# Optimization experiments

Hardware: AMD Instinct MI355X
Metric: run time of the kernel (lower is better)

The kernel has to match this reference:

```python
import jax, jax.numpy as jnp
import numpy as np


def setup_inputs() -> dict:
    key = jax.random.key(0)
    ks = jax.random.split(key, 8)
    B, C, T = 8, 512, 2048
    Cq = C // 8
    s = 0.02
    return {
        "x": jax.random.normal(ks[0], (B, C, T), dtype=jnp.float32),
        "wq": jax.random.normal(ks[1], (Cq, C), dtype=jnp.float32) * s,
        "bq": jax.random.normal(ks[2], (Cq,), dtype=jnp.float32) * s,
        "wk": jax.random.normal(ks[3], (Cq, C), dtype=jnp.float32) * s,
        "bk": jax.random.normal(ks[4], (Cq,), dtype=jnp.float32) * s,
        "wv": jax.random.normal(ks[5], (C, C), dtype=jnp.float32) * s,
        "bv": jax.random.normal(ks[6], (C,), dtype=jnp.float32) * s,
        "gamma": jax.random.normal(ks[7], (1,), dtype=jnp.float32) * s,
    }


def reference(x, wq, bq, wk, bk, wv, bv, gamma):
    # x: [B, C, T]; conv1d with kernel_size=1 == per-timestep linear over channels
    q = jnp.einsum('oc,bct->bto', wq, x) + bq          # [B, T, Cq]
    k = jnp.einsum('oc,bct->bot', wk, x) + bk[None, :, None]  # [B, Cq, T]
    v = jnp.einsum('oc,bct->bto', wv, x) + bv          # [B, T, C]
    attn = jnp.einsum('bto,bos->bts', q, k)            # [B, T, T] (unscaled)
    attn = jax.nn.softmax(attn, axis=-1)
    out = jnp.einsum('bts,bsc->bct', attn, v)          # [B, C, T]
    return gamma[0] * out + x
```

## Files before the change

kernel.cpp:

```cpp
#include <hip/hip_runtime.h>


#define B_ 8
#define C_ 512
#define T_ 2048

typedef __attribute__((ext_vector_type(4))) float f32x4;
typedef __attribute__((ext_vector_type(8))) short bf16x8;
typedef unsigned short u16;
typedef unsigned int u32;

__device__ __forceinline__ u16 f2bf(float f) {
  u32 u = __float_as_uint(f);
  u += 0x7fffu + ((u >> 16) & 1);
  return (u16)(u >> 16);
}
__device__ __forceinline__ float bf2f(u16 h) {
  return __uint_as_float(((u32)h) << 16);
}

extern "C" __global__ __launch_bounds__(256)
void k_wcvt(const float* __restrict__ wq, const float* __restrict__ wk,
            const float* __restrict__ wv, u16* __restrict__ W) {
  int i = blockIdx.x * 256 + threadIdx.x;
  const float* src; u16* dst;
  if (i < 8192)       { src = wq + (size_t)i * 4;            dst = W + (size_t)i * 4; }
  else if (i < 16384) { int j = i - 8192;  src = wk + (size_t)j * 4; dst = W + 32768 + (size_t)j * 4; }
  else                { int j = i - 16384; src = wv + (size_t)j * 4; dst = W + 65536 + (size_t)j * 4; }
  float4 f = *(const float4*)src;
  ushort4 o;
  o.x = f2bf(f.x); o.y = f2bf(f.y); o.z = f2bf(f.z); o.w = f2bf(f.w);
  *(ushort4*)dst = o;
}

extern "C" __global__ __launch_bounds__(256)
void k_xpose(const float* __restrict__ x, u16* __restrict__ xT) {
  __shared__ alignas(16) u16 lds[64 * 72];
  const int tid = threadIdx.x;
  const int t0 = blockIdx.x * 64;
  const int c0 = blockIdx.y * 64;
  const int b  = blockIdx.z;
  const int cr = tid >> 2, tq = tid & 3;
  const float* xp = x + ((size_t)(b * C_ + c0 + cr)) * T_ + t0 + tq * 16;
  u16 vals[16];
#pragma unroll
  for (int q = 0; q < 4; q++) {
    float4 f = *(const float4*)(xp + q * 4);
    vals[q * 4 + 0] = f2bf(f.x);
    vals[q * 4 + 1] = f2bf(f.y);
    vals[q * 4 + 2] = f2bf(f.z);
    vals[q * 4 + 3] = f2bf(f.w);
  }
#pragma unroll
  for (int j = 0; j < 16; j++) lds[(tq * 16 + j) * 72 + cr] = vals[j];
  __syncthreads();
  const int tr = tid >> 2, cq = tid & 3;
  uint4 oa = *(const uint4*)&lds[tr * 72 + cq * 16];
  uint4 ob = *(const uint4*)&lds[tr * 72 + cq * 16 + 8];
  u16* op = xT + ((size_t)(b * T_ + t0 + tr)) * C_ + c0 + cq * 16;
  *(uint4*)op = oa;
  *(uint4*)(op + 8) = ob;
}

extern "C" __global__ __launch_bounds__(256)
void k_qk(const u16* __restrict__ xT, const u16* __restrict__ W,
          const float* __restrict__ bq, const float* __restrict__ bk,
          u16* __restrict__ QK) {
  const int tid = threadIdx.x;
  const int wave = tid >> 6, lane = tid & 63;
  const int quad = lane >> 4, l15 = lane & 15;
  const int id = blockIdx.x;
  const int b  = id & 7;
  const int t0 = (id >> 3) * 32;
  const int n0 = wave * 32;
  f32x4 acc[2][2];
#pragma unroll
  for (int i = 0; i < 2; i++)
#pragma unroll
    for (int j = 0; j < 2; j++) acc[i][j] = (f32x4){0.f, 0.f, 0.f, 0.f};
#pragma unroll
  for (int ks = 0; ks < 16; ks++) {
    bf16x8 af[2], bf[2];
#pragma unroll
    for (int mt = 0; mt < 2; mt++)
      af[mt] = *(const bf16x8*)(xT + ((size_t)(b * T_ + t0 + mt * 16 + l15)) * C_ +
                                ks * 32 + quad * 8);
#pragma unroll
    for (int ntl = 0; ntl < 2; ntl++) {
      const int n = n0 + ntl * 16 + l15;
      const u16* wrow = (n < 64) ? (W + (size_t)n * C_)
                                 : (W + 32768 + (size_t)(n - 64) * C_);
      bf[ntl] = *(const bf16x8*)(wrow + ks * 32 + quad * 8);
    }
#pragma unroll
    for (int mt = 0; mt < 2; mt++)
#pragma unroll
      for (int ntl = 0; ntl < 2; ntl++)
        acc[mt][ntl] = __builtin_amdgcn_mfma_f32_16x16x32_bf16(af[mt], bf[ntl],
                                                               acc[mt][ntl], 0, 0, 0);
  }
#pragma unroll
  for (int ntl = 0; ntl < 2; ntl++) {
    const int n = n0 + ntl * 16 + l15;
    const float bias = (n < 64) ? bq[n] : bk[n - 64];
#pragma unroll
    for (int mt = 0; mt < 2; mt++)
#pragma unroll
      for (int r = 0; r < 4; r++) {
        const int t = t0 + mt * 16 + quad * 4 + r;
        QK[((size_t)(b * T_ + t)) * 128 + n] = f2bf(acc[mt][ntl][r] + bias);
      }
  }
}

extern "C" __global__ __launch_bounds__(256)
void k_vt(const u16* __restrict__ xT, const u16* __restrict__ Wv,
          const float* __restrict__ bv, u16* __restrict__ VT) {
  const int tid = threadIdx.x;
  const int wave = tid >> 6, lane = tid & 63;
  const int quad = lane >> 4, l15 = lane & 15;
  const int id = blockIdx.x;
  const int b   = id & 7;
  const int slot = id >> 3;
  const int tt0 = (slot & 15) * 128;
  const int c00 = (slot >> 4) * 128;
  const int wm = (wave >> 1) * 64, wn = (wave & 1) * 64;
  f32x4 acc[4][4];
#pragma unroll
  for (int i = 0; i < 4; i++)
#pragma unroll
    for (int j = 0; j < 4; j++) acc[i][j] = (f32x4){0.f, 0.f, 0.f, 0.f};

  bf16x8 af[2][4], bfr[2][4];
  auto ldst = [&](int ks, int s) {
#pragma unroll
    for (int mt = 0; mt < 4; mt++)
      af[s][mt] = *(const bf16x8*)(Wv + ((size_t)(c00 + wm + mt * 16 + l15)) * C_ +
                                   ks * 32 + quad * 8);
#pragma unroll
    for (int nt = 0; nt < 4; nt++)
      bfr[s][nt] = *(const bf16x8*)(xT + ((size_t)(b * T_ + tt0 + wn + nt * 16 + l15)) * C_ +
                                    ks * 32 + quad * 8);
  };
  ldst(0, 0);
#pragma unroll
  for (int ks = 0; ks < 16; ks++) {
    const int cur = ks & 1;
    if (ks < 15) ldst(ks + 1, cur ^ 1);
#pragma unroll
    for (int mt = 0; mt < 4; mt++)
#pragma unroll
      for (int nt = 0; nt < 4; nt++)
        acc[mt][nt] = __builtin_amdgcn_mfma_f32_16x16x32_bf16(af[cur][mt], bfr[cur][nt],
                                                              acc[mt][nt], 0, 0, 0);
  }
#pragma unroll
  for (int mt = 0; mt < 4; mt++) {
#pragma unroll
    for (int r = 0; r < 4; r++) {
      const int c = c00 + wm + mt * 16 + quad * 4 + r;
      const float bias = bv[c];
#pragma unroll
      for (int nt = 0; nt < 4; nt++) {
        const int t = tt0 + wn + nt * 16 + l15;
        VT[((size_t)(b * C_ + c)) * T_ + t] = f2bf(acc[mt][nt][r] + bias);
      }
    }
  }
}

extern "C" __global__ __launch_bounds__(256)
void k_attn(const u16* __restrict__ QK, const u16* __restrict__ VT,
            const float* __restrict__ x, const float* __restrict__ gamma,
            float* __restrict__ out) {
  __shared__ alignas(16) u16 Vt[2][256 * 40];
  __shared__ alignas(16) u16 Kt[2][32 * 72];
  __shared__ alignas(16) u16 Pscr[4][32 * 40];

  const int tid = threadIdx.x;
  const int wave = tid >> 6, lane = tid & 63;
  const int quad = lane >> 4, l15 = lane & 15;
  const int id = blockIdx.x;
  const int b  = id & 7;
  const int slot = id >> 3;
  const int c0 = (slot >> 5) * 256;
  const int t0 = (slot & 31) * 64;
  const int wt = wave & 1;
  const int wc = wave >> 1;

  bf16x8 qa[2][2];
#pragma unroll
  for (int mt = 0; mt < 2; mt++) {
    const u16* qp = QK + ((size_t)(b * T_ + t0 + wt * 32 + mt * 16 + l15)) * 128 + quad * 8;
    qa[mt][0] = *(const bf16x8*)qp;
    qa[mt][1] = *(const bf16x8*)(qp + 32);
  }
  f32x4 acc[2][8];
#pragma unroll
  for (int i = 0; i < 2; i++)
#pragma unroll
    for (int j = 0; j < 8; j++) acc[i][j] = (f32x4){0.f, 0.f, 0.f, 0.f};
  float lacc[2][4] = {{0.f, 0.f, 0.f, 0.f}, {0.f, 0.f, 0.f, 0.f}};

  const u16* vbase = VT + ((size_t)(b * C_ + c0)) * T_;
  const u16* kbase = QK + ((size_t)b * T_) * 128 + 64;
  const int vrow = tid >> 2, vch = tid & 3;
  const int krow = tid >> 3, kch = tid & 7;
  uint4 vreg[4];
  uint4 kreg;

  auto gl_tiles = [&](int s0) {
#pragma unroll
    for (int r = 0; r < 4; r++)
      vreg[r] = *(const uint4*)(vbase + ((size_t)(vrow + 64 * r)) * T_ + s0 + vch * 8);
    kreg = *(const uint4*)(kbase + ((size_t)(s0 + krow)) * 128 + kch * 8);
  };
  auto st_tiles = [&](int par) {
#pragma unroll
    for (int r = 0; r < 4; r++)
      *(uint4*)&Vt[par][(vrow + 64 * r) * 40 + vch * 8] = vreg[r];
    *(uint4*)&Kt[par][krow * 72 + kch * 8] = kreg;
  };

  gl_tiles(0);
  st_tiles(0);
  __syncthreads();

  for (int i = 0; i < 64; i++) {
    const int par = i & 1;
    if (i < 63) gl_tiles((i + 1) * 32);

    f32x4 sacc[2][2];
#pragma unroll
    for (int mt = 0; mt < 2; mt++)
#pragma unroll
      for (int nt = 0; nt < 2; nt++) sacc[mt][nt] = (f32x4){0.f, 0.f, 0.f, 0.f};
#pragma unroll
    for (int nt = 0; nt < 2; nt++)
#pragma unroll
      for (int ks = 0; ks < 2; ks++) {
        bf16x8 kb = *(const bf16x8*)&Kt[par][(nt * 16 + l15) * 72 + ks * 32 + quad * 8];
#pragma unroll
        for (int mt = 0; mt < 2; mt++)
          sacc[mt][nt] = __builtin_amdgcn_mfma_f32_16x16x32_bf16(qa[mt][ks], kb,
                                                                sacc[mt][nt], 0, 0, 0);
      }

#pragma unroll
    for (int mt = 0; mt < 2; mt++)
#pragma unroll
      for (int nt = 0; nt < 2; nt++)
#pragma unroll
        for (int r = 0; r < 4; r++) {
          float p = __expf(sacc[mt][nt][r]);
          u16 h = f2bf(p);
          lacc[mt][r] += bf2f(h);
          Pscr[wave][(mt * 16 + quad * 4 + r) * 40 + nt * 16 + l15] = h;
        }
    bf16x8 pa[2];
#pragma unroll
    for (int mt = 0; mt < 2; mt++)
      pa[mt] = *(const bf16x8*)&Pscr[wave][(mt * 16 + l15) * 40 + quad * 8];

#pragma unroll
    for (int nt = 0; nt < 8; nt++) {
      bf16x8 vb = *(const bf16x8*)&Vt[par][(wc * 128 + nt * 16 + l15) * 40 + quad * 8];
#pragma unroll
      for (int mt = 0; mt < 2; mt++)
        acc[mt][nt] = __builtin_amdgcn_mfma_f32_16x16x32_bf16(pa[mt], vb,
                                                              acc[mt][nt], 0, 0, 0);
    }

    if (i < 63) st_tiles(par ^ 1);
    __syncthreads();
  }

#pragma unroll
  for (int mt = 0; mt < 2; mt++)
#pragma unroll
    for (int r = 0; r < 4; r++) {
      float v = lacc[mt][r];
      v += __shfl_xor(v, 1);
      v += __shfl_xor(v, 2);
      v += __shfl_xor(v, 4);
      v += __shfl_xor(v, 8);
      lacc[mt][r] = v;
    }

  const float g = gamma[0];
#pragma unroll
  for (int mt = 0; mt < 2; mt++) {
#pragma unroll
    for (int r = 0; r < 4; r++) {
      const int t = t0 + wt * 32 + mt * 16 + quad * 4 + r;
      const float sc = g / lacc[mt][r];
#pragma unroll
      for (int nt = 0; nt < 8; nt++) {
        const int c = c0 + wc * 128 + nt * 16 + l15;
        const size_t idx = ((size_t)(b * C_ + c)) * T_ + t;
        out[idx] = acc[mt][nt][r] * sc + x[idx];
      }
    }
  }
}

extern "C" void kernel_launch(void* const* d_in, const int* in_sizes, int n_in,
                              void* d_out, int out_size, void* d_ws, size_t ws_size,
                              hipStream_t stream) {
  (void)in_sizes; (void)n_in; (void)out_size; (void)ws_size;
  const float* x  = (const float*)d_in[0];
  const float* wq = (const float*)d_in[1];
  const float* bq = (const float*)d_in[2];
  const float* wk = (const float*)d_in[3];
  const float* bk = (const float*)d_in[4];
  const float* wv = (const float*)d_in[5];
  const float* bv = (const float*)d_in[6];
  const float* gm = (const float*)d_in[7];
  float* out = (float*)d_out;

  u16* xT = (u16*)d_out;
  u16* Wb = (u16*)((char*)d_out + (size_t)17 * 1024 * 1024);
  char* ws = (char*)d_ws;
  u16* QK = (u16*)ws;
  u16* VT = (u16*)(ws + (size_t)4 * 1024 * 1024);

  k_wcvt<<<320, 256, 0, stream>>>(wq, wk, wv, Wb);
  k_xpose<<<dim3(32, 8, 8), 256, 0, stream>>>(x, xT);
  k_qk  <<<512, 256, 0, stream>>>(xT, Wb, bq, bk, QK);
  k_vt  <<<512, 256, 0, stream>>>(xT, Wb + 65536, bv, VT);
  k_attn<<<512, 256, 0, stream>>>(QK, VT, x, gm, out);
}
```

Measured before the change: 297.2 us.

## Load K and V fragments directly from global memory, dropping LDS staging and barriers

The attention kernel no longer stages K and V tiles through double-buffered shared memory with block-wide barriers. Each wave now loads its own MFMA operand fragments straight from global memory (relying on cache), prefetches the next K fragment in registers, and the launch bounds request two blocks per CU. This removes LDS traffic and __syncthreads. In exchange, each wave issues redundant global loads (the two waves sharing wc load the same V, the K tile is loaded by all four waves), the V loads for each iteration are issued without prefetch ahead of use, and register pressure rises.

```diff
diff --git a/kernel.cpp b/kernel.cpp
--- a/kernel.cpp
+++ b/kernel.cpp
@@ -169,12 +169,10 @@
   }
 }
 
-extern "C" __global__ __launch_bounds__(256)
+extern "C" __global__ __launch_bounds__(256, 2)
 void k_attn(const u16* __restrict__ QK, const u16* __restrict__ VT,
             const float* __restrict__ x, const float* __restrict__ gamma,
             float* __restrict__ out) {
-  __shared__ alignas(16) u16 Vt[2][256 * 40];
-  __shared__ alignas(16) u16 Kt[2][32 * 72];
   __shared__ alignas(16) u16 Pscr[4][32 * 40];
 
   const int tid = threadIdx.x;
@@ -202,33 +200,29 @@
     for (int j = 0; j < 8; j++) acc[i][j] = (f32x4){0.f, 0.f, 0.f, 0.f};
   float lacc[2][4] = {{0.f, 0.f, 0.f, 0.f}, {0.f, 0.f, 0.f, 0.f}};
 
-  const u16* vbase = VT + ((size_t)(b * C_ + c0)) * T_;
-  const u16* kbase = QK + ((size_t)b * T_) * 128 + 64;
-  const int vrow = tid >> 2, vch = tid & 3;
-  const int krow = tid >> 3, kch = tid & 7;
-  uint4 vreg[4];
-  uint4 kreg;
-
-  auto gl_tiles = [&](int s0) {
-#pragma unroll
-    for (int r = 0; r < 4; r++)
-      vreg[r] = *(const uint4*)(vbase + ((size_t)(vrow + 64 * r)) * T_ + s0 + vch * 8);
-    kreg = *(const uint4*)(kbase + ((size_t)(s0 + krow)) * 128 + kch * 8);
-  };
-  auto st_tiles = [&](int par) {
-#pragma unroll
-    for (int r = 0; r < 4; r++)
-      *(uint4*)&Vt[par][(vrow + 64 * r) * 40 + vch * 8] = vreg[r];
-    *(uint4*)&Kt[par][krow * 72 + kch * 8] = kreg;
-  };
-
-  gl_tiles(0);
-  st_tiles(0);
-  __syncthreads();
+  const u16* kp = QK + ((size_t)(b * T_ + l15)) * 128 + 64 + quad * 8;
+  const u16* vp = VT + ((size_t)(b * C_ + c0 + wc * 128 + l15)) * T_ + quad * 8;
+
+  bf16x8 kbf[2][2];
+#pragma unroll
+  for (int nt = 0; nt < 2; nt++)
+#pragma unroll
+    for (int ks = 0; ks < 2; ks++)
+      kbf[nt][ks] = *(const bf16x8*)(kp + ((nt * 16) << 7) + ks * 32);
 
   for (int i = 0; i < 64; i++) {
-    const int par = i & 1;
-    if (i < 63) gl_tiles((i + 1) * 32);
+    bf16x8 vbf[8];
+#pragma unroll
+    for (int nt = 0; nt < 8; nt++)
+      vbf[nt] = *(const bf16x8*)(vp + ((size_t)nt << 15) + i * 32);
+
+    const int inx = (i < 63) ? i + 1 : i;
+    bf16x8 kbn[2][2];
+#pragma unroll
+    for (int nt = 0; nt < 2; nt++)
+#pragma unroll
+      for (int ks = 0; ks < 2; ks++)
+        kbn[nt][ks] = *(const bf16x8*)(kp + ((inx * 32 + nt * 16) << 7) + ks * 32);
 
     f32x4 sacc[2][2];
 #pragma unroll
@@ -238,13 +232,11 @@
 #pragma unroll
     for (int nt = 0; nt < 2; nt++)
 #pragma unroll
-      for (int ks = 0; ks < 2; ks++) {
-        bf16x8 kb = *(const bf16x8*)&Kt[par][(nt * 16 + l15) * 72 + ks * 32 + quad * 8];
+      for (int ks = 0; ks < 2; ks++)
 #pragma unroll
         for (int mt = 0; mt < 2; mt++)
-          sacc[mt][nt] = __builtin_amdgcn_mfma_f32_16x16x32_bf16(qa[mt][ks], kb,
-                                                                sacc[mt][nt], 0, 0, 0);
-      }
+          sacc[mt][nt] = __builtin_amdgcn_mfma_f32_16x16x32_bf16(qa[mt][ks], kbf[nt][ks],
+                                                                 sacc[mt][nt], 0, 0, 0);
 
 #pragma unroll
     for (int mt = 0; mt < 2; mt++)
@@ -263,16 +255,17 @@
       pa[mt] = *(const bf16x8*)&Pscr[wave][(mt * 16 + l15) * 40 + quad * 8];
 
 #pragma unroll
-    for (int nt = 0; nt < 8; nt++) {
-      bf16x8 vb = *(const bf16x8*)&Vt[par][(wc * 128 + nt * 16 + l15) * 40 + quad * 8];
+    for (int nt = 0; nt < 8; nt++)
 #pragma unroll
       for (int mt = 0; mt < 2; mt++)
-        acc[mt][nt] = __builtin_amdgcn_mfma_f32_16x16x32_bf16(pa[mt], vb,
+        acc[mt][nt] = __builtin_amdgcn_mfma_f32_16x16x32_bf16(pa[mt], vbf[nt],
                                                               acc[mt][nt], 0, 0, 0);
-    }
-
-    if (i < 63) st_tiles(par ^ 1);
-    __syncthreads();
+
+#pragma unroll
+    for (int nt = 0; nt < 2; nt++)
+#pragma unroll
+      for (int ks = 0; ks < 2; ks++)
+        kbf[nt][ks] = kbn[nt][ks];
   }
 
 #pragma unroll
```

New measurement: 329.9 us. 1.11x slower.

## Keep K and P in registers, transpose S MFMA, drop LDS scratch

Applied to the files above, without the earlier changes.

Removes the K tile and P scratch from shared memory. K fragments are loaded straight from global memory into registers and prefetched one step ahead. The QK^T MFMA operands are swapped so the score tile comes out transposed, and P is repacked into the PV A-operand with cross-lane shuffles instead of an LDS round trip. Exponentials are packed to bf16 with v_cvt_pk_bf16_f32, and the row sums are reduced across quads at the end. This cuts LDS traffic and barriers-bound work, at the cost of more shuffles and direct global K loads that are redundant across waves.

```diff
diff --git a/kernel.cpp b/kernel.cpp
--- a/kernel.cpp
+++ b/kernel.cpp
@@ -174,8 +174,6 @@
             const float* __restrict__ x, const float* __restrict__ gamma,
             float* __restrict__ out) {
   __shared__ alignas(16) u16 Vt[2][256 * 40];
-  __shared__ alignas(16) u16 Kt[2][32 * 72];
-  __shared__ alignas(16) u16 Pscr[4][32 * 40];
 
   const int tid = threadIdx.x;
   const int wave = tid >> 6, lane = tid & 63;
@@ -187,11 +185,12 @@
   const int t0 = (slot & 31) * 64;
   const int wt = wave & 1;
   const int wc = wave >> 1;
+  const int t0w = t0 + wt * 32;
 
   bf16x8 qa[2][2];
 #pragma unroll
   for (int mt = 0; mt < 2; mt++) {
-    const u16* qp = QK + ((size_t)(b * T_ + t0 + wt * 32 + mt * 16 + l15)) * 128 + quad * 8;
+    const u16* qp = QK + ((size_t)(b * T_ + t0w + mt * 16 + l15)) * 128 + quad * 8;
     qa[mt][0] = *(const bf16x8*)qp;
     qa[mt][1] = *(const bf16x8*)(qp + 32);
   }
@@ -200,32 +199,39 @@
   for (int i = 0; i < 2; i++)
 #pragma unroll
     for (int j = 0; j < 8; j++) acc[i][j] = (f32x4){0.f, 0.f, 0.f, 0.f};
-  float lacc[2][4] = {{0.f, 0.f, 0.f, 0.f}, {0.f, 0.f, 0.f, 0.f}};
-
+  float lsum[2] = {0.f, 0.f};
+
+  const u16* kp = QK + ((size_t)(b * T_ + l15)) * 128 + 64 + quad * 8;
   const u16* vbase = VT + ((size_t)(b * C_ + c0)) * T_;
-  const u16* kbase = QK + ((size_t)b * T_) * 128 + 64;
   const int vrow = tid >> 2, vch = tid & 3;
-  const int krow = tid >> 3, kch = tid & 7;
   uint4 vreg[4];
-  uint4 kreg;
 
   auto gl_tiles = [&](int s0) {
 #pragma unroll
     for (int r = 0; r < 4; r++)
       vreg[r] = *(const uint4*)(vbase + ((size_t)(vrow + 64 * r)) * T_ + s0 + vch * 8);
-    kreg = *(const uint4*)(kbase + ((size_t)(s0 + krow)) * 128 + kch * 8);
   };
   auto st_tiles = [&](int par) {
 #pragma unroll
     for (int r = 0; r < 4; r++)
       *(uint4*)&Vt[par][(vrow + 64 * r) * 40 + vch * 8] = vreg[r];
-    *(uint4*)&Kt[par][krow * 72 + kch * 8] = kreg;
   };
+
+  bf16x8 kbf[2][2];
+#pragma unroll
+  for (int nt = 0; nt < 2; nt++)
+#pragma unroll
+    for (int ks = 0; ks < 2; ks++)
+      kbf[nt][ks] = *(const bf16x8*)(kp + ((nt * 16) << 7) + ks * 32);
 
   gl_tiles(0);
   st_tiles(0);
   __syncthreads();
 
+  const int srcA = ((quad & 1) << 5) + l15;
+  const int srcB = srcA + 16;
+  const bool hiq = quad >= 2;
+
   for (int i = 0; i < 64; i++) {
     const int par = i & 1;
     if (i < 63) gl_tiles((i + 1) * 32);
@@ -238,29 +244,55 @@
 #pragma unroll
     for (int nt = 0; nt < 2; nt++)
 #pragma unroll
-      for (int ks = 0; ks < 2; ks++) {
-        bf16x8 kb = *(const bf16x8*)&Kt[par][(nt * 16 + l15) * 72 + ks * 32 + quad * 8];
+      for (int ks = 0; ks < 2; ks++)
 #pragma unroll
         for (int mt = 0; mt < 2; mt++)
-          sacc[mt][nt] = __builtin_amdgcn_mfma_f32_16x16x32_bf16(qa[mt][ks], kb,
-                                                                sacc[mt][nt], 0, 0, 0);
+          sacc[mt][nt] = __builtin_amdgcn_mfma_f32_16x16x32_bf16(kbf[nt][ks], qa[mt][ks],
+                                                                 sacc[mt][nt], 0, 0, 0);
+
+    const int inx = (i < 63) ? i + 1 : 63;
+#pragma unroll
+    for (int nt = 0; nt < 2; nt++)
+#pragma unroll
+      for (int ks = 0; ks < 2; ks++)
+        kbf[nt][ks] = *(const bf16x8*)(kp + ((inx * 32 + nt * 16) << 7) + ks * 32);
+
+    u32 pk[2][2][2];
+#pragma unroll
+    for (int mt = 0; mt < 2; mt++)
+#pragma unroll
+      for (int nt = 0; nt < 2; nt++) {
+        float p0 = __expf(sacc[mt][nt][0]);
+        float p1 = __expf(sacc[mt][nt][1]);
+        float p2 = __expf(sacc[mt][nt][2]);
+        float p3 = __expf(sacc[mt][nt][3]);
+        u32 w01, w23;
+        asm("v_cvt_pk_bf16_f32 %0, %1, %2" : "=v"(w01) : "v"(p0), "v"(p1));
+        asm("v_cvt_pk_bf16_f32 %0, %1, %2" : "=v"(w23) : "v"(p2), "v"(p3));
+        pk[mt][nt][0] = w01;
+        pk[mt][nt][1] = w23;
+        lsum[mt] += __uint_as_float(w01 << 16) + __uint_as_float(w01 & 0xffff0000u);
+        lsum[mt] += __uint_as_float(w23 << 16) + __uint_as_float(w23 & 0xffff0000u);
       }
 
-#pragma unroll
-    for (int mt = 0; mt < 2; mt++)
-#pragma unroll
-      for (int nt = 0; nt < 2; nt++)
-#pragma unroll
-        for (int r = 0; r < 4; r++) {
-          float p = __expf(sacc[mt][nt][r]);
-          u16 h = f2bf(p);
-          lacc[mt][r] += bf2f(h);
-          Pscr[wave][(mt * 16 + quad * 4 + r) * 40 + nt * 16 + l15] = h;
-        }
     bf16x8 pa[2];
 #pragma unroll
-    for (int mt = 0; mt < 2; mt++)
-      pa[mt] = *(const bf16x8*)&Pscr[wave][(mt * 16 + l15) * 40 + quad * 8];
+    for (int mt = 0; mt < 2; mt++) {
+      int a0 = __shfl((int)pk[mt][0][0], srcA);
+      int a1 = __shfl((int)pk[mt][0][1], srcA);
+      int b0 = __shfl((int)pk[mt][0][0], srcB);
+      int b1 = __shfl((int)pk[mt][0][1], srcB);
+      int c0_ = __shfl((int)pk[mt][1][0], srcA);
+      int c1_ = __shfl((int)pk[mt][1][1], srcA);
+      int d0 = __shfl((int)pk[mt][1][0], srcB);
+      int d1 = __shfl((int)pk[mt][1][1], srcB);
+      union { bf16x8 v; int w[4]; } pu;
+      pu.w[0] = hiq ? c0_ : a0;
+      pu.w[1] = hiq ? c1_ : a1;
+      pu.w[2] = hiq ? d0 : b0;
+      pu.w[3] = hiq ? d1 : b1;
+      pa[mt] = pu.v;
+    }
 
 #pragma unroll
     for (int nt = 0; nt < 8; nt++) {
@@ -276,24 +308,21 @@
   }
 
 #pragma unroll
-  for (int mt = 0; mt < 2; mt++)
+  for (int mt = 0; mt < 2; mt++) {
+    float v = lsum[mt];
+    v += __shfl_xor(v, 16);
+    v += __shfl_xor(v, 32);
+    lsum[mt] = v;
+  }
+
+  const float g = gamma[0];
+#pragma unroll
+  for (int mt = 0; mt < 2; mt++) {
 #pragma unroll
     for (int r = 0; r < 4; r++) {
-      float v = lacc[mt][r];
-      v += __shfl_xor(v, 1);
-      v += __shfl_xor(v, 2);
-      v += __shfl_xor(v, 4);
-      v += __shfl_xor(v, 8);
-      lacc[mt][r] = v;
-    }
-
-  const float g = gamma[0];
-#pragma unroll
-  for (int mt = 0; mt < 2; mt++) {
-#pragma unroll
-    for (int r = 0; r < 4; r++) {
-      const int t = t0 + wt * 32 + mt * 16 + quad * 4 + r;
-      const float sc = g / lacc[mt][r];
+      const int t = t0w + mt * 16 + quad * 4 + r;
+      const float denom = __shfl(lsum[mt], quad * 4 + r);
+      const float sc = g / denom;
 #pragma unroll
       for (int nt = 0; nt < 8; nt++) {
         const int c = c0 + wc * 128 + nt * 16 + l15;
```

New measurement: 356.6 us. 20.0% more time.

## Compute softmax row sums via MFMA with ones and use packed bf16 convert

Applied to the files above, without the earlier changes.

Replaces the per-element scalar accumulation of exp values, and the final cross-lane shuffle reduction, with an extra MFMA per row tile that multiplies the bf16 P fragment by a vector of ones. The exp-to-bf16 rounding now uses the hardware packed convert instruction instead of manual integer rounding. The K tile row stride in shared memory is padded from 72 to 88 to change the bank mapping. This trades some VALU work for a few extra matrix instructions per iteration and slightly more LDS.

```diff
diff --git a/kernel.cpp b/kernel.cpp
--- a/kernel.cpp
+++ b/kernel.cpp
@@ -174,7 +174,7 @@
             const float* __restrict__ x, const float* __restrict__ gamma,
             float* __restrict__ out) {
   __shared__ alignas(16) u16 Vt[2][256 * 40];
-  __shared__ alignas(16) u16 Kt[2][32 * 72];
+  __shared__ alignas(16) u16 Kt[2][32 * 88];
   __shared__ alignas(16) u16 Pscr[4][32 * 40];
 
   const int tid = threadIdx.x;
@@ -200,7 +200,12 @@
   for (int i = 0; i < 2; i++)
 #pragma unroll
     for (int j = 0; j < 8; j++) acc[i][j] = (f32x4){0.f, 0.f, 0.f, 0.f};
-  float lacc[2][4] = {{0.f, 0.f, 0.f, 0.f}, {0.f, 0.f, 0.f, 0.f}};
+  f32x4 acc1[2];
+  acc1[0] = (f32x4){0.f, 0.f, 0.f, 0.f};
+  acc1[1] = (f32x4){0.f, 0.f, 0.f, 0.f};
+  bf16x8 ones;
+#pragma unroll
+  for (int j = 0; j < 8; j++) ones[j] = (short)0x3F80;
 
   const u16* vbase = VT + ((size_t)(b * C_ + c0)) * T_;
   const u16* kbase = QK + ((size_t)b * T_) * 128 + 64;
@@ -219,7 +224,7 @@
 #pragma unroll
     for (int r = 0; r < 4; r++)
       *(uint4*)&Vt[par][(vrow + 64 * r) * 40 + vch * 8] = vreg[r];
-    *(uint4*)&Kt[par][krow * 72 + kch * 8] = kreg;
+    *(uint4*)&Kt[par][krow * 88 + kch * 8] = kreg;
   };
 
   gl_tiles(0);
@@ -239,7 +244,7 @@
     for (int nt = 0; nt < 2; nt++)
 #pragma unroll
       for (int ks = 0; ks < 2; ks++) {
-        bf16x8 kb = *(const bf16x8*)&Kt[par][(nt * 16 + l15) * 72 + ks * 32 + quad * 8];
+        bf16x8 kb = *(const bf16x8*)&Kt[par][(nt * 16 + l15) * 88 + ks * 32 + quad * 8];
 #pragma unroll
         for (int mt = 0; mt < 2; mt++)
           sacc[mt][nt] = __builtin_amdgcn_mfma_f32_16x16x32_bf16(qa[mt][ks], kb,
@@ -249,18 +254,29 @@
 #pragma unroll
     for (int mt = 0; mt < 2; mt++)
 #pragma unroll
-      for (int nt = 0; nt < 2; nt++)
-#pragma unroll
-        for (int r = 0; r < 4; r++) {
-          float p = __expf(sacc[mt][nt][r]);
-          u16 h = f2bf(p);
-          lacc[mt][r] += bf2f(h);
-          Pscr[wave][(mt * 16 + quad * 4 + r) * 40 + nt * 16 + l15] = h;
-        }
+      for (int nt = 0; nt < 2; nt++) {
+        float p0 = __expf(sacc[mt][nt][0]);
+        float p1 = __expf(sacc[mt][nt][1]);
+        float p2 = __expf(sacc[mt][nt][2]);
+        float p3 = __expf(sacc[mt][nt][3]);
+        u32 w01, w23;
+        asm("v_cvt_pk_bf16_f32 %0, %1, %2" : "=v"(w01) : "v"(p0), "v"(p1));
+        asm("v_cvt_pk_bf16_f32 %0, %1, %2" : "=v"(w23) : "v"(p2), "v"(p3));
+        u16* pr = &Pscr[wave][(mt * 16 + quad * 4) * 40 + nt * 16 + l15];
+        pr[0]   = (u16)w01;
+        pr[40]  = (u16)(w01 >> 16);
+        pr[80]  = (u16)w23;
+        pr[120] = (u16)(w23 >> 16);
+      }
     bf16x8 pa[2];
 #pragma unroll
     for (int mt = 0; mt < 2; mt++)
       pa[mt] = *(const bf16x8*)&Pscr[wave][(mt * 16 + l15) * 40 + quad * 8];
+
+#pragma unroll
+    for (int mt = 0; mt < 2; mt++)
+      acc1[mt] = __builtin_amdgcn_mfma_f32_16x16x32_bf16(pa[mt], ones,
+                                                         acc1[mt], 0, 0, 0);
 
 #pragma unroll
     for (int nt = 0; nt < 8; nt++) {
@@ -275,25 +291,13 @@
     __syncthreads();
   }
 
-#pragma unroll
-  for (int mt = 0; mt < 2; mt++)
-#pragma unroll
-    for (int r = 0; r < 4; r++) {
-      float v = lacc[mt][r];
-      v += __shfl_xor(v, 1);
-      v += __shfl_xor(v, 2);
-      v += __shfl_xor(v, 4);
-      v += __shfl_xor(v, 8);
-      lacc[mt][r] = v;
-    }
-
   const float g = gamma[0];
 #pragma unroll
   for (int mt = 0; mt < 2; mt++) {
 #pragma unroll
     for (int r = 0; r < 4; r++) {
       const int t = t0 + wt * 32 + mt * 16 + quad * 4 + r;
-      const float sc = g / lacc[mt][r];
+      const float sc = g / acc1[mt][r];
 #pragma unroll
       for (int nt = 0; nt < 8; nt++) {
         const int c = c0 + wc * 128 + nt * 16 + l15;
```

Result: no change. 300.7 us (+1.2%).
